# Kernel tuning notes

Hardware: AMD Instinct MI355X
Metric: run time of the kernel (lower is better)

Reference implementation:

```python
import jax, jax.numpy as jnp
import numpy as np
from jax import lax

B, C, L = 4, 4, 32000
F3, K, STRIDE = 1536, 16, 8  # encoder emits 3*N feats; N = F3//3 = 512


def setup_inputs() -> dict:
    key = jax.random.key(0)
    k1, k2 = jax.random.split(key)
    x = jax.random.normal(k1, (B, C, L), dtype=jnp.float32)
    # one Conv1d(1, F3, K, stride) weight per channel coder: [C, F3, 1, K]
    W = jax.random.normal(k2, (C, F3, 1, K), dtype=jnp.float32) * 0.05
    return {"x": x, "W": W}


def _conv1d(xc, wc):
    # xc: [B, L] single-channel waveform; wc: [F3, 1, K]
    y = lax.conv_general_dilated(
        xc[:, None, :], wc, window_strides=(STRIDE,), padding="VALID",
        dimension_numbers=("NCH", "OIH", "NCH"))
    return y  # [B, F3, T]


def reference(x, W):
    # per-channel coders, vectorized over the channel axis -> [B, C, F3, T]
    feat = jax.vmap(_conv1d, in_axes=(1, 0), out_axes=1)(x, W)
    k, q, v = jnp.split(feat, 3, axis=-2)  # each [B, C, N, T]
    # w[b,i,j,t] = sum_f k[b,j,f,t] * q[b,i,f,t]  (i = query channel, j = key channel)
    w = jnp.einsum("bjft,bift->bijt", k, q)
    w = jax.nn.softmax(w, axis=2)  # softmax over key-channel axis (torch dim 2)
    out = (jnp.einsum("bijt,bjft->bift", w, v) + v) * 0.5
    return out  # [B, C, N, T]
```

## Files before the change

### kernel.cpp

```cpp
#include <hip/hip_runtime.h>


#define BB 4
#define CC 4
#define LL 32000
#define KK 16
#define ST 8
#define NN 512
#define TT 3999
#define F3 1536
#define FC 16

__global__ __launch_bounds__(256) void k0_M(const float* __restrict__ W,
                                            float* __restrict__ M) {
  const int i = blockIdx.x >> 2, j = blockIdx.x & 3;
  __shared__ float wq[NN * KK];
  __shared__ float wk[NN * KK];
  const int baseq = (i * F3 + NN) * KK;
  const int basek = (j * F3) * KK;
  for (int idx = threadIdx.x; idx < NN * KK; idx += 256) {
    wq[idx] = W[baseq + idx];
    wk[idx] = W[basek + idx];
  }
  __syncthreads();
  const int k = threadIdx.x >> 4, k2 = threadIdx.x & 15;
  float acc = 0.f;
  for (int f = 0; f < NN; ++f)
    acc = fmaf(wq[f * KK + k], wk[f * KK + k2], acc);
  M[((i * 4 + j) * 16 + k) * 16 + k2] = acc;
}

template <int I>
__device__ __forceinline__ void k1_row(const float xr[4][16],
                                       const float* __restrict__ M,
                                       float* __restrict__ A, int bb, int t) {
  float w[4];
#pragma unroll
  for (int j = 0; j < 4; ++j) {
    const float* Mp = M + (I * 4 + j) * 256;
    float acc = 0.f;
#pragma unroll
    for (int k = 0; k < 16; ++k) {
      float y = 0.f;
#pragma unroll
      for (int k2 = 0; k2 < 16; ++k2)
        y = fmaf(Mp[k * 16 + k2], xr[j][k2], y);
      acc = fmaf(xr[I][k], y, acc);
    }
    w[j] = acc;
  }
  const float m = fmaxf(fmaxf(w[0], w[1]), fmaxf(w[2], w[3]));
  const float e0 = __expf(w[0] - m), e1 = __expf(w[1] - m);
  const float e2 = __expf(w[2] - m), e3 = __expf(w[3] - m);
  const float inv = 0.5f / (e0 + e1 + e2 + e3);
  float4 av;
  av.x = e0 * inv;
  av.y = e1 * inv;
  av.z = e2 * inv;
  av.w = e3 * inv;
  if (I == 0) av.x += 0.5f;
  if (I == 1) av.y += 0.5f;
  if (I == 2) av.z += 0.5f;
  if (I == 3) av.w += 0.5f;
  *reinterpret_cast<float4*>(A + ((bb * TT + t) * 4 + I) * 4) = av;
}

__global__ __launch_bounds__(256, 4) void k1_A(const float* __restrict__ x,
                                               const float* __restrict__ M,
                                               float* __restrict__ A) {
  const int bb = blockIdx.y;
  const int lane = threadIdx.x & 63;
  const int wv = threadIdx.x >> 6;
  const int t = blockIdx.x * 64 + lane;
  if (t >= TT) return;
  float xr[4][16];
#pragma unroll
  for (int c = 0; c < 4; ++c) {
    const float* xp = x + (bb * CC + c) * LL + t * ST;
#pragma unroll
    for (int k4 = 0; k4 < 16; k4 += 4) {
      const float4 v4 = *reinterpret_cast<const float4*>(xp + k4);
      xr[c][k4 + 0] = v4.x;
      xr[c][k4 + 1] = v4.y;
      xr[c][k4 + 2] = v4.z;
      xr[c][k4 + 3] = v4.w;
    }
  }
  if (wv == 0)      k1_row<0>(xr, M, A, bb, t);
  else if (wv == 1) k1_row<1>(xr, M, A, bb, t);
  else if (wv == 2) k1_row<2>(xr, M, A, bb, t);
  else              k1_row<3>(xr, M, A, bb, t);
}

__global__ __launch_bounds__(256, 4) void k2_out(const float* __restrict__ x,
                                                 const float* __restrict__ W,
                                                 const float* __restrict__ A,
                                                 float* __restrict__ out) {
  const int bb = blockIdx.x >> 4;
  const int t = (blockIdx.x & 15) * 256 + (int)threadIdx.x;
  const int f0 = blockIdx.y * FC;
  if (t >= TT) return;
  float xr[4][16];
#pragma unroll
  for (int c = 0; c < 4; ++c) {
    const float* xp = x + (bb * CC + c) * LL + t * ST;
#pragma unroll
    for (int k4 = 0; k4 < 16; k4 += 4) {
      const float4 v4 = *reinterpret_cast<const float4*>(xp + k4);
      xr[c][k4 + 0] = v4.x;
      xr[c][k4 + 1] = v4.y;
      xr[c][k4 + 2] = v4.z;
      xr[c][k4 + 3] = v4.w;
    }
  }
  float4 a[4];
  {
    const float4* ap = reinterpret_cast<const float4*>(A + (bb * TT + t) * 16);
#pragma unroll
    for (int i = 0; i < 4; ++i) a[i] = ap[i];
  }

#pragma unroll 2
  for (int f = 0; f < FC; ++f) {
    const int fg = f0 + f;
    const float* w0 = W + (0 * F3 + 2 * NN + fg) * KK;
    const float* w1 = W + (1 * F3 + 2 * NN + fg) * KK;
    const float* w2 = W + (2 * F3 + 2 * NN + fg) * KK;
    const float* w3 = W + (3 * F3 + 2 * NN + fg) * KK;
    float v0 = 0.f, v1 = 0.f, v2 = 0.f, v3 = 0.f;
#pragma unroll
    for (int k = 0; k < 16; ++k) {
      v0 = fmaf(w0[k], xr[0][k], v0);
      v1 = fmaf(w1[k], xr[1][k], v1);
      v2 = fmaf(w2[k], xr[2][k], v2);
      v3 = fmaf(w3[k], xr[3][k], v3);
    }
#pragma unroll
    for (int i = 0; i < 4; ++i) {
      const float o =
          fmaf(a[i].w, v3, fmaf(a[i].z, v2, fmaf(a[i].y, v1, a[i].x * v0)));
      out[((bb * 4 + i) * NN + fg) * TT + t] = o;
    }
  }
}

extern "C" void kernel_launch(void* const* d_in, const int* in_sizes, int n_in,
                              void* d_out, int out_size, void* d_ws,
                              size_t ws_size, hipStream_t stream) {
  const float* x = (const float*)d_in[0];
  const float* W = (const float*)d_in[1];
  float* out = (float*)d_out;
  float* Mws = (float*)d_ws;
  float* Aws = Mws + 4 * 4 * 16 * 16;

  hipLaunchKernelGGL(k0_M, dim3(16), dim3(256), 0, stream, W, Mws);
  hipLaunchKernelGGL(k1_A, dim3(63, BB), dim3(256), 0, stream, x, Mws, Aws);
  hipLaunchKernelGGL(k2_out, dim3(64, 32), dim3(256), 0, stream, x, W, Aws, out);
}
```

Before: 60.11 us.

## Transpose k2 outputs through LDS for float4 stores and double features per block

Each wave now computes four features at a time and transposes the results through a per-wave shared-memory buffer. Each lane then writes four consecutive time steps with one float4 store instead of one scalar store per feature. FC is doubled to 32, with launch bounds lowered to 3, so each block reuses its loaded x window and attention coefficients over more features. Because TT is odd, the float4 stores are not 16-byte aligned, and the transpose adds LDS traffic and register pressure.

```diff
diff --git a/kernel.cpp b/kernel.cpp
--- a/kernel.cpp
+++ b/kernel.cpp
@@ -9,7 +9,7 @@
 #define NN 512
 #define TT 3999
 #define F3 1536
-#define FC 16
+#define FC 32
 
 __global__ __launch_bounds__(256) void k0_M(const float* __restrict__ W,
                                             float* __restrict__ M) {
@@ -92,18 +92,24 @@
   else              k1_row<3>(xr, M, A, bb, t);
 }
 
-__global__ __launch_bounds__(256, 4) void k2_out(const float* __restrict__ x,
+__global__ __launch_bounds__(256, 3) void k2_out(const float* __restrict__ x,
                                                  const float* __restrict__ W,
                                                  const float* __restrict__ A,
                                                  float* __restrict__ out) {
+  __shared__ float tbuf[4][256];
+  const int tid = (int)threadIdx.x;
+  const int ln = tid & 63;
+  const int wv = tid >> 6;
   const int bb = blockIdx.x >> 4;
-  const int t = (blockIdx.x & 15) * 256 + (int)threadIdx.x;
+  const int t0w = (blockIdx.x & 15) * 256 + wv * 64;
   const int f0 = blockIdx.y * FC;
-  if (t >= TT) return;
+  const int t = t0w + ln;
+  const int tcl = min(t, TT - 1);
+
   float xr[4][16];
 #pragma unroll
   for (int c = 0; c < 4; ++c) {
-    const float* xp = x + (bb * CC + c) * LL + t * ST;
+    const float* xp = x + (bb * CC + c) * LL + tcl * ST;
 #pragma unroll
     for (int k4 = 0; k4 < 16; k4 += 4) {
       const float4 v4 = *reinterpret_cast<const float4*>(xp + k4);
@@ -115,31 +121,60 @@
   }
   float4 a[4];
   {
-    const float4* ap = reinterpret_cast<const float4*>(A + (bb * TT + t) * 16);
+    const float4* ap =
+        reinterpret_cast<const float4*>(A + (bb * TT + tcl) * 16);
 #pragma unroll
     for (int i = 0; i < 4; ++i) a[i] = ap[i];
   }
 
-#pragma unroll 2
-  for (int f = 0; f < FC; ++f) {
-    const int fg = f0 + f;
-    const float* w0 = W + (0 * F3 + 2 * NN + fg) * KK;
-    const float* w1 = W + (1 * F3 + 2 * NN + fg) * KK;
-    const float* w2 = W + (2 * F3 + 2 * NN + fg) * KK;
-    const float* w3 = W + (3 * F3 + 2 * NN + fg) * KK;
-    float v0 = 0.f, v1 = 0.f, v2 = 0.f, v3 = 0.f;
+  const int fprow = ln >> 4;
+  const int tq = (ln & 15) * 4;
+  const int tg = t0w + tq;
+
+  for (int g = 0; g < FC / 4; ++g) {
+    float o[4][4];
 #pragma unroll
-    for (int k = 0; k < 16; ++k) {
-      v0 = fmaf(w0[k], xr[0][k], v0);
-      v1 = fmaf(w1[k], xr[1][k], v1);
-      v2 = fmaf(w2[k], xr[2][k], v2);
-      v3 = fmaf(w3[k], xr[3][k], v3);
+    for (int fj = 0; fj < 4; ++fj) {
+      const int fg = f0 + g * 4 + fj;
+      const float* w0 = W + (0 * F3 + 2 * NN + fg) * KK;
+      const float* w1 = W + (1 * F3 + 2 * NN + fg) * KK;
+      const float* w2 = W + (2 * F3 + 2 * NN + fg) * KK;
+      const float* w3 = W + (3 * F3 + 2 * NN + fg) * KK;
+      float v0 = 0.f, v1 = 0.f, v2 = 0.f, v3 = 0.f;
+#pragma unroll
+      for (int k = 0; k < 16; ++k) {
+        v0 = fmaf(w0[k], xr[0][k], v0);
+        v1 = fmaf(w1[k], xr[1][k], v1);
+        v2 = fmaf(w2[k], xr[2][k], v2);
+        v3 = fmaf(w3[k], xr[3][k], v3);
+      }
+#pragma unroll
+      for (int i = 0; i < 4; ++i)
+        o[i][fj] = fmaf(a[i].w, v3,
+                        fmaf(a[i].z, v2, fmaf(a[i].y, v1, a[i].x * v0)));
     }
+
+    float4 tr[4];
 #pragma unroll
     for (int i = 0; i < 4; ++i) {
-      const float o =
-          fmaf(a[i].w, v3, fmaf(a[i].z, v2, fmaf(a[i].y, v1, a[i].x * v0)));
-      out[((bb * 4 + i) * NN + fg) * TT + t] = o;
+      tbuf[wv][0 * 64 + ln] = o[i][0];
+      tbuf[wv][1 * 64 + ln] = o[i][1];
+      tbuf[wv][2 * 64 + ln] = o[i][2];
+      tbuf[wv][3 * 64 + ln] = o[i][3];
+      tr[i] = *reinterpret_cast<const float4*>(&tbuf[wv][fprow * 64 + tq]);
+    }
+
+#pragma unroll
+    for (int i = 0; i < 4; ++i) {
+      const int row = ((bb * 4 + i) * NN + f0 + g * 4 + fprow);
+      float* op = out + (size_t)row * TT + tg;
+      if (tg + 3 < TT) {
+        *reinterpret_cast<float4*>(op) = tr[i];
+      } else {
+        if (tg + 0 < TT) op[0] = tr[i].x;
+        if (tg + 1 < TT) op[1] = tr[i].y;
+        if (tg + 2 < TT) op[2] = tr[i].z;
+      }
     }
   }
 }
@@ -155,5 +190,6 @@
 
   hipLaunchKernelGGL(k0_M, dim3(16), dim3(256), 0, stream, W, Mws);
   hipLaunchKernelGGL(k1_A, dim3(63, BB), dim3(256), 0, stream, x, Mws, Aws);
-  hipLaunchKernelGGL(k2_out, dim3(64, 32), dim3(256), 0, stream, x, W, Aws, out);
+  hipLaunchKernelGGL(k2_out, dim3(BB * 16, NN / FC), dim3(256), 0, stream, x,
+                     W, Aws, out);
 }
```

Result: slower. 65.16 us (+8.4%).

## Stage k2 output through shared memory for aligned float4 stores

Applied to the files above, without the earlier changes.

The output kernel now writes each group of 8 feature rows into an LDS buffer. Each stored row is shifted by a per-row offset so that the row start, which sits at a multiple of TT=3999, lines up with 16-byte boundaries. Each wave then writes aligned float4 stores, with scalar code for the misaligned head and tail elements, in place of per-thread scalar stores. Feature channels per block double from 16 to 32, which halves the grid's y dimension and amortises the x and A loads over more outputs. The price is two block barriers per group, LDS usage, and more complex edge handling.

```diff
diff --git a/kernel.cpp b/kernel.cpp
--- a/kernel.cpp
+++ b/kernel.cpp
@@ -9,7 +9,9 @@
 #define NN 512
 #define TT 3999
 #define F3 1536
-#define FC 16
+#define FC 32
+#define FG 8
+#define TROW 260
 
 __global__ __launch_bounds__(256) void k0_M(const float* __restrict__ W,
                                             float* __restrict__ M) {
@@ -96,14 +98,20 @@
                                                  const float* __restrict__ W,
                                                  const float* __restrict__ A,
                                                  float* __restrict__ out) {
+  __shared__ float ob[FG][4][TROW];
+  const int tid = (int)threadIdx.x;
+  const int ln = tid & 63, wv = tid >> 6;
   const int bb = blockIdx.x >> 4;
-  const int t = (blockIdx.x & 15) * 256 + (int)threadIdx.x;
+  const int t0 = (blockIdx.x & 15) * 256;
   const int f0 = blockIdx.y * FC;
-  if (t >= TT) return;
+  const int t = t0 + tid;
+  const int tcl = min(t, TT - 1);
+  const int nvalid = min(256, TT - t0);
+
   float xr[4][16];
 #pragma unroll
   for (int c = 0; c < 4; ++c) {
-    const float* xp = x + (bb * CC + c) * LL + t * ST;
+    const float* xp = x + (bb * CC + c) * LL + tcl * ST;
 #pragma unroll
     for (int k4 = 0; k4 < 16; k4 += 4) {
       const float4 v4 = *reinterpret_cast<const float4*>(xp + k4);
@@ -115,32 +123,84 @@
   }
   float4 a[4];
   {
-    const float4* ap = reinterpret_cast<const float4*>(A + (bb * TT + t) * 16);
+    const float4* ap =
+        reinterpret_cast<const float4*>(A + (bb * TT + tcl) * 16);
 #pragma unroll
     for (int i = 0; i < 4; ++i) a[i] = ap[i];
   }
 
-#pragma unroll 2
-  for (int f = 0; f < FC; ++f) {
-    const int fg = f0 + f;
-    const float* w0 = W + (0 * F3 + 2 * NN + fg) * KK;
-    const float* w1 = W + (1 * F3 + 2 * NN + fg) * KK;
-    const float* w2 = W + (2 * F3 + 2 * NN + fg) * KK;
-    const float* w3 = W + (3 * F3 + 2 * NN + fg) * KK;
-    float v0 = 0.f, v1 = 0.f, v2 = 0.f, v3 = 0.f;
-#pragma unroll
-    for (int k = 0; k < 16; ++k) {
-      v0 = fmaf(w0[k], xr[0][k], v0);
-      v1 = fmaf(w1[k], xr[1][k], v1);
-      v2 = fmaf(w2[k], xr[2][k], v2);
-      v3 = fmaf(w3[k], xr[3][k], v3);
-    }
-#pragma unroll
-    for (int i = 0; i < 4; ++i) {
-      const float o =
-          fmaf(a[i].w, v3, fmaf(a[i].z, v2, fmaf(a[i].y, v1, a[i].x * v0)));
-      out[((bb * 4 + i) * NN + fg) * TT + t] = o;
-    }
+  for (int g = 0; g < FC / FG; ++g) {
+#pragma unroll
+    for (int fs = 0; fs < FG; ++fs) {
+      const int fg = f0 + g * FG + fs;
+      const float* w0 = W + (0 * F3 + 2 * NN + fg) * KK;
+      const float* w1 = W + (1 * F3 + 2 * NN + fg) * KK;
+      const float* w2 = W + (2 * F3 + 2 * NN + fg) * KK;
+      const float* w3 = W + (3 * F3 + 2 * NN + fg) * KK;
+      float v0 = 0.f, v1 = 0.f, v2 = 0.f, v3 = 0.f;
+#pragma unroll
+      for (int k = 0; k < 16; ++k) {
+        v0 = fmaf(w0[k], xr[0][k], v0);
+        v1 = fmaf(w1[k], xr[1][k], v1);
+        v2 = fmaf(w2[k], xr[2][k], v2);
+        v3 = fmaf(w3[k], xr[3][k], v3);
+      }
+      const int s = (-fs) & 3;
+#pragma unroll
+      for (int i = 0; i < 4; ++i) {
+        const float o =
+            fmaf(a[i].w, v3, fmaf(a[i].z, v2, fmaf(a[i].y, v1, a[i].x * v0)));
+        ob[fs][i][tid + s] = o;
+      }
+    }
+    asm volatile("s_waitcnt lgkmcnt(0)" ::: "memory");
+    __builtin_amdgcn_s_barrier();
+
+#pragma unroll
+    for (int rr = 0; rr < 8; ++rr) {
+      const int fs = wv * 2 + (rr >> 2);
+      const int ii = rr & 3;
+      const int fg = f0 + g * FG + fs;
+      const size_t rb = (size_t)((bb * 4 + ii) * NN + fg) * TT + t0;
+      float* op = out + rb;
+      const int head = fs & 3;
+      if (head == 0) {
+        const int tl = 4 * ln;
+        const float4 v = *reinterpret_cast<const float4*>(&ob[fs][ii][tl]);
+        if (tl + 3 < nvalid) {
+          *reinterpret_cast<float4*>(op + tl) = v;
+        } else {
+          if (tl + 0 < nvalid) op[tl + 0] = v.x;
+          if (tl + 1 < nvalid) op[tl + 1] = v.y;
+          if (tl + 2 < nvalid) op[tl + 2] = v.z;
+        }
+      } else {
+        if (ln < 63) {
+          const int tl = head + 4 * ln;
+          const float4 v =
+              *reinterpret_cast<const float4*>(&ob[fs][ii][4 * ln + 4]);
+          if (tl + 3 < nvalid) {
+            *reinterpret_cast<float4*>(op + tl) = v;
+          } else {
+            if (tl + 0 < nvalid) op[tl + 0] = v.x;
+            if (tl + 1 < nvalid) op[tl + 1] = v.y;
+            if (tl + 2 < nvalid) op[tl + 2] = v.z;
+          }
+        } else {
+          const int s = 4 - head;
+#pragma unroll
+          for (int d = 0; d < 3; ++d)
+            if (d < head) op[d] = ob[fs][ii][d + s];
+#pragma unroll
+          for (int d = 0; d < 3; ++d) {
+            const int tl = head + 252 + d;
+            if (d < 4 - head && tl < nvalid) op[tl] = ob[fs][ii][tl + s];
+          }
+        }
+      }
+    }
+    asm volatile("s_waitcnt lgkmcnt(0)" ::: "memory");
+    __builtin_amdgcn_s_barrier();
   }
 }
 
@@ -155,5 +215,6 @@
 
   hipLaunchKernelGGL(k0_M, dim3(16), dim3(256), 0, stream, W, Mws);
   hipLaunchKernelGGL(k1_A, dim3(63, BB), dim3(256), 0, stream, x, Mws, Aws);
-  hipLaunchKernelGGL(k2_out, dim3(64, 32), dim3(256), 0, stream, x, W, Aws, out);
-}
+  hipLaunchKernelGGL(k2_out, dim3(BB * 16, NN / FC), dim3(256), 0, stream, x,
+                     W, Aws, out);
+}
```

Measured after the change: 68.75 us. 14.4% more time.
